# Optimization experiments

Measured on AMD Instinct MI355X. Metric: run time of the kernel, lower is better.

## Reference

```python
import jax, jax.numpy as jnp
import numpy as np

N_NODES = 100000
N_EDGES = 1600000
HIDDEN = 64
NUM_GRAPHS = 512


def setup_inputs() -> dict:
    key = jax.random.key(0)
    k1, k2, k3, k4, k5, k6 = jax.random.split(key, 6)
    x = jax.random.normal(k1, (N_NODES, HIDDEN), dtype=jnp.float32)
    edge_index = jax.random.randint(k2, (2, N_EDGES), 0, N_NODES, dtype=jnp.int64)
    batch = jnp.sort(jax.random.randint(k3, (N_NODES,), 0, NUM_GRAPHS, dtype=jnp.int64))
    # SAGPooling's internal GraphConv(64 -> 1): lin_rel (with bias) on aggregated
    # neighbor features, lin_root (no bias) on self features.
    s = 1.0 / np.sqrt(HIDDEN)
    W_rel = jax.random.uniform(k4, (HIDDEN, 1), dtype=jnp.float32, minval=-s, maxval=s)
    b_rel = jax.random.uniform(k5, (1,), dtype=jnp.float32, minval=-s, maxval=s)
    W_root = jax.random.uniform(k6, (HIDDEN, 1), dtype=jnp.float32, minval=-s, maxval=s)
    return {"x": x, "edge_index": edge_index, "batch": batch,
            "W_rel": W_rel, "b_rel": b_rel, "W_root": W_root}


def reference(x, edge_index, batch, W_rel, b_rel, W_root):
    n = x.shape[0]
    src, dst = edge_index[0], edge_index[1]
    # GraphConv (aggr='add'): sum x_j over in-edges, then lin_rel(aggr)+lin_root(x)
    aggr = jax.ops.segment_sum(x[src], dst, num_segments=n)          # [N, H]
    score = (aggr @ W_rel + b_rel + x @ W_root)[:, 0]                # [N]
    # min_score=-1 -> scores softmax-normalized per graph; all nodes kept in order
    m = jax.ops.segment_max(score, batch, num_segments=NUM_GRAPHS)   # [G]
    e = jnp.exp(score - m[batch])
    z = jax.ops.segment_sum(e, batch, num_segments=NUM_GRAPHS)       # [G]
    att = e / z[batch]                                               # [N]
    att_x = x * att[:, None]                                         # [N, H]
    # global_add_pool
    return jax.ops.segment_sum(att_x, batch, num_segments=NUM_GRAPHS)  # [G, H]
```

## Files before the change

### kernel.cpp

```cpp
#include <hip/hip_runtime.h>
#include <math.h>
#include <stdint.h>


#define H 64
#define TILE 4096
#define NTHR_S 1024
#define EPT (TILE / NTHR_S)
#define BUCKET_SZ 256
#define MAX_NB 400
#define NREP 8
#define SUBCAP 768
#define CAP (NREP * SUBCAP)
#define ROWS_PER_WAVE 32
#define PSCALE 16384.0f
#define INV_PSCALE 6.103515625e-05f

__global__ __launch_bounds__(256) void node_prep(
    const float4* __restrict__ x4, const float4* __restrict__ W_rel4,
    const float4* __restrict__ W_root4,
    float* __restrict__ p, float* __restrict__ r,
    float* __restrict__ num, float* __restrict__ z,
    unsigned int* __restrict__ cursor,
    int n_nodes, int num_elems, int n_graphs, int nb)
{
    int gid = (int)(blockIdx.x * blockDim.x + threadIdx.x);
    if (gid < num_elems) num[gid] = 0.0f;
    else if (gid < num_elems + n_graphs) z[gid - num_elems] = 0.0f;
    else if (gid < num_elems + n_graphs + nb * NREP) {
        int idx = gid - num_elems - n_graphs;
        int rep = idx / nb;
        int k   = idx - rep * nb;
        cursor[idx] = (unsigned int)(k * CAP + rep * SUBCAP);
    }

    int node = blockIdx.x * 64 + (threadIdx.x >> 2);
    int q    = threadIdx.x & 3;
    if (node >= n_nodes) return;

    float pv = 0.0f, rv = 0.0f;
    #pragma unroll
    for (int kk = 0; kk < 4; ++kk) {
        float4 v  = x4[node * 16 + kk * 4 + q];
        float4 wr = W_rel4[kk * 4 + q];
        float4 wo = W_root4[kk * 4 + q];
        pv += v.x * wr.x + v.y * wr.y + v.z * wr.z + v.w * wr.w;
        rv += v.x * wo.x + v.y * wo.y + v.z * wo.z + v.w * wo.w;
    }
    pv += __shfl_xor(pv, 1, 64); pv += __shfl_xor(pv, 2, 64);
    rv += __shfl_xor(rv, 1, 64); rv += __shfl_xor(rv, 2, 64);
    if (q == 0) { p[node] = pv; r[node] = rv; }
}

__global__ __launch_bounds__(NTHR_S) void edge_sort(
    const int* __restrict__ src, const int* __restrict__ dst,
    const float* __restrict__ p,
    unsigned int* __restrict__ cursor, unsigned int* __restrict__ sorted_g,
    int n_edges, int nb)
{
    __shared__ unsigned int hist[MAX_NB];
    __shared__ unsigned int offs[MAX_NB];
    __shared__ unsigned int gbase[MAX_NB];
    __shared__ unsigned int wtot[8];
    __shared__ unsigned int svals[TILE];
    __shared__ unsigned short sbid[TILE];

    int b = blockIdx.x;
    int rep = b & (NREP - 1);
    int base = b * TILE;
    int tile_n = min(TILE, n_edges - base);
    int tid = threadIdx.x;

    if (tid < nb) hist[tid] = 0;
    __syncthreads();

    unsigned int dd[EPT]; int ss[EPT];
    float pv[EPT];
    unsigned int bk[EPT], pk[EPT], slot[EPT];

    int j0 = tid * EPT;
    if (j0 + EPT <= tile_n) {
        int4 s4 = *(const int4*)(src + base + j0);
        int4 d4 = *(const int4*)(dst + base + j0);
        ss[0] = s4.x; ss[1] = s4.y; ss[2] = s4.z; ss[3] = s4.w;
        dd[0] = (unsigned int)d4.x; dd[1] = (unsigned int)d4.y;
        dd[2] = (unsigned int)d4.z; dd[3] = (unsigned int)d4.w;
    } else {
        #pragma unroll
        for (int u = 0; u < EPT; ++u) {
            int j = j0 + u;
            if (j < tile_n) { ss[u] = src[base + j];
                              dd[u] = (unsigned int)dst[base + j]; }
            else dd[u] = 0xFFFFFFFFu;
        }
    }
    #pragma unroll
    for (int u = 0; u < EPT; ++u)
        if (dd[u] != 0xFFFFFFFFu) pv[u] = p[ss[u]];
    #pragma unroll
    for (int u = 0; u < EPT; ++u) {
        if (dd[u] != 0xFFFFFFFFu) {
            bk[u] = dd[u] >> 8;
            int q = (int)__float2int_rn(pv[u] * PSCALE);
            q = max(-8388607, min(8388607, q));
            pk[u] = ((unsigned int)q << 8) | (dd[u] & 255u);
            slot[u] = atomicAdd(&hist[bk[u]], 1u);
        }
    }
    __syncthreads();

    int wv = tid >> 6, ln = tid & 63;
    unsigned int v = 0, xs = 0;
    if (wv < 7) {
        int bin = wv * 64 + ln;
        v = (bin < nb) ? hist[bin] : 0;
        xs = v;
        #pragma unroll
        for (int off = 1; off < 64; off <<= 1) {
            unsigned int y = __shfl_up(xs, off, 64);
            if (ln >= off) xs += y;
        }
        if (ln == 63) wtot[wv] = xs;
    }
    __syncthreads();
    if (wv < 7) {
        int bin = wv * 64 + ln;
        unsigned int pre = 0;
        #pragma unroll
        for (int w2 = 0; w2 < 7; ++w2)
            pre += (w2 < wv) ? wtot[w2] : 0u;
        if (bin < nb) {
            offs[bin]  = pre + xs - v;
            gbase[bin] = v ? atomicAdd(&cursor[rep * nb + bin], v) : 0u;
        }
    }
    __syncthreads();

    #pragma unroll
    for (int u = 0; u < EPT; ++u) {
        if (dd[u] != 0xFFFFFFFFu) {
            unsigned int pos = offs[bk[u]] + slot[u];
            svals[pos] = pk[u];
            sbid[pos]  = (unsigned short)bk[u];
        }
    }
    __syncthreads();

    for (int j = tid; j < tile_n; j += NTHR_S) {
        unsigned int bb = sbid[j];
        unsigned int gi = gbase[bb] + ((unsigned int)j - offs[bb]);
        unsigned int lim = bb * (unsigned int)CAP
                         + (unsigned int)(rep + 1) * SUBCAP;
        if (gi < lim)
            sorted_g[gi] = svals[j];
    }
}

__global__ __launch_bounds__(256) void bucket_accum(
    const unsigned int* __restrict__ sorted_g,
    const unsigned int* __restrict__ cursor,
    const float* __restrict__ r,
    float* __restrict__ e_buf, int n_nodes, int nb)
{
    __shared__ int acc[BUCKET_SZ];
    __shared__ unsigned int cnts[NREP];
    int k = blockIdx.x;
    int tid = threadIdx.x;
    acc[tid] = 0;
    if (tid < NREP) {
        unsigned int begr = (unsigned int)(k * CAP + tid * SUBCAP);
        cnts[tid] = min(cursor[tid * nb + k] - begr, (unsigned int)SUBCAP);
    }
    __syncthreads();

    #pragma unroll
    for (int rp = 0; rp < NREP; ++rp) {
        unsigned int beg = (unsigned int)(k * CAP + rp * SUBCAP);
        unsigned int cnt = cnts[rp];
        unsigned int n4  = cnt & ~3u;
        for (unsigned int j = tid * 4; j < n4; j += 1024) {
            uint4 v = *(const uint4*)(sorted_g + beg + j);
            atomicAdd(&acc[v.x & 255u], (int)v.x >> 8);
            atomicAdd(&acc[v.y & 255u], (int)v.y >> 8);
            atomicAdd(&acc[v.z & 255u], (int)v.z >> 8);
            atomicAdd(&acc[v.w & 255u], (int)v.w >> 8);
        }
        for (unsigned int j = n4 + tid; j < cnt; j += 256) {
            unsigned int v = sorted_g[beg + j];
            atomicAdd(&acc[v & 255u], (int)v >> 8);
        }
    }
    __syncthreads();

    int node = k * BUCKET_SZ + tid;
    if (node < n_nodes)
        e_buf[node] = __expf((float)acc[tid] * INV_PSCALE + r[node]);
}

__global__ __launch_bounds__(256) void pool(
    const float* __restrict__ x, const float* __restrict__ e_buf,
    const int* __restrict__ batch,
    float* __restrict__ num, float* __restrict__ z, int n_nodes)
{
    int wid = threadIdx.x >> 6, lane = threadIdx.x & 63;
    int row0 = (blockIdx.x * 4 + wid) * ROWS_PER_WAVE;
    if (row0 >= n_nodes) return;
    int rend = min(row0 + ROWS_PER_WAVE, n_nodes);

    int g_first = batch[row0];
    int g_last  = batch[rend - 1];

    if (g_first == g_last && rend - row0 == ROWS_PER_WAVE) {
        float acc = 0.0f, acce = 0.0f;
        #pragma unroll 8
        for (int u = 0; u < ROWS_PER_WAVE; ++u) {
            int i = row0 + u;
            float e = e_buf[i];
            acc  += x[i * H + lane] * e;
            acce += e;
        }
        unsafeAtomicAdd(&num[g_first * H + lane], acc);
        if (lane == 0) unsafeAtomicAdd(&z[g_first], acce);
        return;
    }

    int cur_g = g_first;
    float acc = 0.0f, acce = 0.0f;
    for (int i = row0; i < rend; ++i) {
        int g = batch[i];
        if (g != cur_g) {
            unsafeAtomicAdd(&num[cur_g * H + lane], acc);
            if (lane == 0) unsafeAtomicAdd(&z[cur_g], acce);
            acc = 0.0f; acce = 0.0f;
            cur_g = g;
        }
        float e = e_buf[i];
        acc  += x[i * H + lane] * e;
        acce += e;
    }
    unsafeAtomicAdd(&num[cur_g * H + lane], acc);
    if (lane == 0) unsafeAtomicAdd(&z[cur_g], acce);
}

__global__ __launch_bounds__(256) void finalize(
    const float* __restrict__ num, const float* __restrict__ z,
    float* __restrict__ out, int num_elems)
{
    int i = (int)(blockIdx.x * blockDim.x + threadIdx.x);
    if (i >= num_elems) return;
    float zz = z[i >> 6];
    out[i] = (zz != 0.0f) ? num[i] / zz : 0.0f;
}

extern "C" void kernel_launch(void* const* d_in, const int* in_sizes, int n_in,
                              void* d_out, int out_size, void* d_ws, size_t ws_size,
                              hipStream_t stream)
{
    const float* x      = (const float*)d_in[0];
    const int*   eidx   = (const int*)d_in[1];
    const int*   batch  = (const int*)d_in[2];
    const float* W_rel  = (const float*)d_in[3];
    const float* W_root = (const float*)d_in[5];
    float* out = (float*)d_out;

    const int n_nodes  = in_sizes[0] / H;
    const int n_edges  = in_sizes[1] / 2;
    const int n_graphs = out_size / H;
    const int nb     = (n_nodes + BUCKET_SZ - 1) / BUCKET_SZ;
    const int ntiles = (n_edges + TILE - 1) / TILE;

    const int* src = eidx;
    const int* dst = eidx + n_edges;

    float* p     = (float*)d_ws;
    float* r     = p + n_nodes;
    float* e_buf = r + n_nodes;
    float* z     = e_buf + n_nodes;
    float* num   = z + n_graphs;
    unsigned int* cursor = (unsigned int*)(num + out_size);
    uintptr_t raw = (uintptr_t)(cursor + nb * NREP);
    unsigned int* sorted_g = (unsigned int*)((raw + 15) & ~(uintptr_t)15);

    int np_blocks = (n_nodes + 63) / 64;
    node_prep<<<np_blocks, 256, 0, stream>>>(
        (const float4*)x, (const float4*)W_rel, (const float4*)W_root,
        p, r, num, z, cursor, n_nodes, out_size, n_graphs, nb);
    edge_sort<<<ntiles, NTHR_S, 0, stream>>>(src, dst, p, cursor, sorted_g,
                                             n_edges, nb);
    bucket_accum<<<nb, 256, 0, stream>>>(sorted_g, cursor, r, e_buf, n_nodes, nb);
    pool<<<(n_nodes + 4 * ROWS_PER_WAVE - 1) / (4 * ROWS_PER_WAVE), 256, 0, stream>>>(
        x, e_buf, batch, num, z, n_nodes);
    finalize<<<(out_size + 255) / 256, 256, 0, stream>>>(num, z, out, out_size);
}
```

Baseline: 125.6 us.

## Fuse bucket accumulation and attention pooling into one kernel

```diff
diff --git a/kernel.cpp b/kernel.cpp
--- a/kernel.cpp
+++ b/kernel.cpp
@@ -12,7 +12,6 @@
 #define NREP 8
 #define SUBCAP 768
 #define CAP (NREP * SUBCAP)
-#define ROWS_PER_WAVE 32
 #define PSCALE 16384.0f
 #define INV_PSCALE 6.103515625e-05f
 
@@ -156,17 +155,30 @@
     }
 }
 
-__global__ __launch_bounds__(256) void bucket_accum(
+__global__ __launch_bounds__(512) void bucket_pool(
     const unsigned int* __restrict__ sorted_g,
     const unsigned int* __restrict__ cursor,
     const float* __restrict__ r,
-    float* __restrict__ e_buf, int n_nodes, int nb)
+    const float* __restrict__ x,
+    const int* __restrict__ batch,
+    float* __restrict__ num, float* __restrict__ z,
+    int n_nodes, int nb)
 {
     __shared__ int acc[BUCKET_SZ];
+    __shared__ float e_lds[BUCKET_SZ];
+    __shared__ int g_lds[BUCKET_SZ];
     __shared__ unsigned int cnts[NREP];
+
     int k = blockIdx.x;
     int tid = threadIdx.x;
-    acc[tid] = 0;
+    int node0 = k * BUCKET_SZ;
+
+    if (tid < BUCKET_SZ) acc[tid] = 0;
+    else {
+        int t2 = tid - BUCKET_SZ;
+        int node = node0 + t2;
+        g_lds[t2] = (node < n_nodes) ? batch[node] : -1;
+    }
     if (tid < NREP) {
         unsigned int begr = (unsigned int)(k * CAP + tid * SUBCAP);
         cnts[tid] = min(cursor[tid * nb + k] - begr, (unsigned int)SUBCAP);
@@ -178,67 +190,64 @@
         unsigned int beg = (unsigned int)(k * CAP + rp * SUBCAP);
         unsigned int cnt = cnts[rp];
         unsigned int n4  = cnt & ~3u;
-        for (unsigned int j = tid * 4; j < n4; j += 1024) {
+        for (unsigned int j = tid * 4; j < n4; j += 2048) {
             uint4 v = *(const uint4*)(sorted_g + beg + j);
             atomicAdd(&acc[v.x & 255u], (int)v.x >> 8);
             atomicAdd(&acc[v.y & 255u], (int)v.y >> 8);
             atomicAdd(&acc[v.z & 255u], (int)v.z >> 8);
             atomicAdd(&acc[v.w & 255u], (int)v.w >> 8);
         }
-        for (unsigned int j = n4 + tid; j < cnt; j += 256) {
+        for (unsigned int j = n4 + tid; j < cnt; j += 512) {
             unsigned int v = sorted_g[beg + j];
             atomicAdd(&acc[v & 255u], (int)v >> 8);
         }
     }
     __syncthreads();
 
-    int node = k * BUCKET_SZ + tid;
-    if (node < n_nodes)
-        e_buf[node] = __expf((float)acc[tid] * INV_PSCALE + r[node]);
-}
-
-__global__ __launch_bounds__(256) void pool(
-    const float* __restrict__ x, const float* __restrict__ e_buf,
-    const int* __restrict__ batch,
-    float* __restrict__ num, float* __restrict__ z, int n_nodes)
-{
-    int wid = threadIdx.x >> 6, lane = threadIdx.x & 63;
-    int row0 = (blockIdx.x * 4 + wid) * ROWS_PER_WAVE;
+    if (tid < BUCKET_SZ) {
+        int node = node0 + tid;
+        e_lds[tid] = (node < n_nodes)
+                   ? __expf((float)acc[tid] * INV_PSCALE + r[node]) : 0.0f;
+    }
+    __syncthreads();
+
+    int wid = tid >> 6, lane = tid & 63;
+    int l0 = wid * 32;
+    int row0 = node0 + l0;
     if (row0 >= n_nodes) return;
-    int rend = min(row0 + ROWS_PER_WAVE, n_nodes);
-
-    int g_first = batch[row0];
-    int g_last  = batch[rend - 1];
-
-    if (g_first == g_last && rend - row0 == ROWS_PER_WAVE) {
-        float acc = 0.0f, acce = 0.0f;
+    int rend = min(row0 + 32, n_nodes);
+
+    int g_first = g_lds[l0];
+    int g_last  = g_lds[rend - 1 - node0];
+
+    if (g_first == g_last && rend - row0 == 32) {
+        float acc_f = 0.0f, acce = 0.0f;
         #pragma unroll 8
-        for (int u = 0; u < ROWS_PER_WAVE; ++u) {
-            int i = row0 + u;
-            float e = e_buf[i];
-            acc  += x[i * H + lane] * e;
-            acce += e;
-        }
-        unsafeAtomicAdd(&num[g_first * H + lane], acc);
+        for (int u = 0; u < 32; ++u) {
+            float e = e_lds[l0 + u];
+            acc_f += x[(row0 + u) * H + lane] * e;
+            acce  += e;
+        }
+        unsafeAtomicAdd(&num[g_first * H + lane], acc_f);
         if (lane == 0) unsafeAtomicAdd(&z[g_first], acce);
         return;
     }
 
     int cur_g = g_first;
-    float acc = 0.0f, acce = 0.0f;
+    float acc_f = 0.0f, acce = 0.0f;
     for (int i = row0; i < rend; ++i) {
-        int g = batch[i];
+        int g = g_lds[i - node0];
         if (g != cur_g) {
-            unsafeAtomicAdd(&num[cur_g * H + lane], acc);
+            unsafeAtomicAdd(&num[cur_g * H + lane], acc_f);
             if (lane == 0) unsafeAtomicAdd(&z[cur_g], acce);
-            acc = 0.0f; acce = 0.0f;
+            acc_f = 0.0f; acce = 0.0f;
             cur_g = g;
         }
-        float e = e_buf[i];
-        acc  += x[i * H + lane] * e;
-        acce += e;
-    }
-    unsafeAtomicAdd(&num[cur_g * H + lane], acc);
+        float e = e_lds[i - node0];
+        acc_f += x[i * H + lane] * e;
+        acce  += e;
+    }
+    unsafeAtomicAdd(&num[cur_g * H + lane], acc_f);
     if (lane == 0) unsafeAtomicAdd(&z[cur_g], acce);
 }
 
@@ -274,8 +283,7 @@
 
     float* p     = (float*)d_ws;
     float* r     = p + n_nodes;
-    float* e_buf = r + n_nodes;
-    float* z     = e_buf + n_nodes;
+    float* z     = r + n_nodes;
     float* num   = z + n_graphs;
     unsigned int* cursor = (unsigned int*)(num + out_size);
     uintptr_t raw = (uintptr_t)(cursor + nb * NREP);
@@ -287,8 +295,7 @@
         p, r, num, z, cursor, n_nodes, out_size, n_graphs, nb);
     edge_sort<<<ntiles, NTHR_S, 0, stream>>>(src, dst, p, cursor, sorted_g,
                                              n_edges, nb);
-    bucket_accum<<<nb, 256, 0, stream>>>(sorted_g, cursor, r, e_buf, n_nodes, nb);
-    pool<<<(n_nodes + 4 * ROWS_PER_WAVE - 1) / (4 * ROWS_PER_WAVE), 256, 0, stream>>>(
-        x, e_buf, batch, num, z, n_nodes);
+    bucket_pool<<<nb, 512, 0, stream>>>(sorted_g, cursor, r, x, batch,
+                                        num, z, n_nodes, nb);
     finalize<<<(out_size + 255) / 256, 256, 0, stream>>>(num, z, out, out_size);
 }
```

Measured after the change: 118.5 us. 1.06x faster.
